# Performance work log

Hardware: AMD Instinct MI355X
Metric: run time of the kernel (lower is better)

Reference implementation:

```python
import jax, jax.numpy as jnp
import numpy as np

T, S, D, W = 256, 512, 640, 64  # tasks, n_support, feat_dim, n_way

def setup_inputs() -> dict:
    key = jax.random.key(0)
    k1, = jax.random.split(key, 1)
    support = jax.random.normal(k1, (T, S, D), dtype=jnp.float32)
    # balanced labels: each class appears exactly S // W times per task
    support_labels = jnp.tile(jnp.arange(S, dtype=jnp.int64) % W, (T, 1))
    return {
        "support": support,
        "support_labels": support_labels,
        "n_way": W,
        "target_pos": jnp.ones((1,), dtype=jnp.float32),
        "target_neg": jnp.zeros((1,), dtype=jnp.float32),
    }

def reference(support, support_labels, n_way, target_pos, target_neg):
    tasks, n_support, _ = support.shape
    # [T, W, S] one-hot (class x support sample)
    one_hot_label = jax.nn.one_hot(support_labels, n_way, dtype=support.dtype)
    one_hot_label = jnp.transpose(one_hot_label, (0, 2, 1))
    # per-class feature sums: [T, W, D] (segment-sum expressed as matmul, as in source)
    pos_feat = jnp.einsum('tws,tsd->twd', one_hot_label, support)
    neg_feat = jnp.sum(support, axis=1, keepdims=True) - pos_feat
    k_shot = jnp.sum(one_hot_label, axis=-1).reshape(tasks, n_way, 1)  # [T, W, 1]
    pos_feat = pos_feat / k_shot
    neg_feat = neg_feat / (n_support - k_shot)
    ff = jnp.sum(pos_feat * pos_feat, axis=2, keepdims=True)
    bb = jnp.sum(neg_feat * neg_feat, axis=2, keepdims=True)
    fb = jnp.sum(pos_feat * neg_feat, axis=2, keepdims=True)
    den = jnp.clip(ff * bb - fb * fb, 1e-06, None)
    fg_scale = target_pos * bb - target_neg * fb
    bg_scale = target_pos * fb - target_neg * ff
    weights = (fg_scale * pos_feat - bg_scale * neg_feat) / den
    return weights
```

## Files before the change

kernel.cpp:

```cpp
#include <hip/hip_runtime.h>

#define T_  256
#define S_  512
#define D_  640
#define W_  64
#define D4  (D_/4)
#define KSH (S_/W_)

static __device__ __forceinline__ float4 f4add(float4 a, float4 b) {
    return make_float4(a.x + b.x, a.y + b.y, a.z + b.z, a.w + b.w);
}

__global__ __launch_bounds__(S_) void k0_build_idx(const int* __restrict__ labels,
                                                   int* __restrict__ idx,
                                                   int* __restrict__ kshot) {
    __shared__ int cnt[W_];
    const int t   = blockIdx.x;
    const int tid = threadIdx.x;
    if (tid < W_) cnt[tid] = 0;
    __syncthreads();
    const int lab  = labels[t * S_ + tid];
    const int slot = atomicAdd(&cnt[lab], 1);
    if (slot < KSH) idx[t * S_ + lab * KSH + slot] = tid;
    __syncthreads();
    if (tid < W_) kshot[t * W_ + tid] = cnt[tid];
}

__global__ __launch_bounds__(320) void k1_pos_sums(const float4* __restrict__ sup4,
                                                   const int* __restrict__ idx,
                                                   const int* __restrict__ kshot,
                                                   float4* __restrict__ out4) {
    const int b   = blockIdx.x;
    const int t   = b / (W_ / 2);
    const int wp  = b % (W_ / 2);
    const int tid = threadIdx.x;
    const int wl  = (tid >= D4) ? 1 : 0;
    const int q   = tid - wl * D4;
    const int w   = wp * 2 + wl;

    const int*    myidx = idx + t * S_ + w * KSH;
    const float4* base  = sup4 + (size_t)t * S_ * D4;
    int ks = kshot[t * W_ + w];
    if (ks > KSH) ks = KSH;

    float4 acc = make_float4(0.f, 0.f, 0.f, 0.f);
    for (int k = 0; k < ks; ++k) {
        const int s = myidx[k];
        acc = f4add(acc, base[(size_t)s * D4 + q]);
    }
    out4[((size_t)t * W_ + w) * D4 + q] = acc;
}

__global__ __launch_bounds__(256) void k2_totals(const float4* __restrict__ pos4,
                                                 float4* __restrict__ tot4) {
    const int gid = blockIdx.x * blockDim.x + threadIdx.x;
    if (gid >= T_ * D4) return;
    const int t = gid / D4;
    const int q = gid - t * D4;
    const float4* base = pos4 + (size_t)t * W_ * D4 + q;
    float4 acc = make_float4(0.f, 0.f, 0.f, 0.f);
#pragma unroll 8
    for (int w = 0; w < W_; ++w) acc = f4add(acc, base[(size_t)w * D4]);
    tot4[gid] = acc;
}

__global__ __launch_bounds__(64) void k3_final(float4* __restrict__ out4,
                                               const float4* __restrict__ tot4,
                                               const int* __restrict__ kshot,
                                               const float* __restrict__ tp_,
                                               const float* __restrict__ tn_) {
    const int b    = blockIdx.x;
    const int t    = b / W_;
    const int w    = b - t * W_;
    const int lane = threadIdx.x;

    const float tp  = tp_[0];
    const float tn  = tn_[0];
    const float ksf = (float)kshot[t * W_ + w];
    const float nkf = (float)S_ - ksf;

    float4 pv[3], nv[3];
    float ff = 0.f, bb = 0.f, fb = 0.f;

#pragma unroll
    for (int r = 0; r < 3; ++r) {
        const int q = lane + r * 64;
        if (q < D4) {
            const float4 p  = out4[((size_t)t * W_ + w) * D4 + q];
            const float4 tv = tot4[(size_t)t * D4 + q];
            float4 pos, neg;
            pos.x = p.x / ksf;  pos.y = p.y / ksf;
            pos.z = p.z / ksf;  pos.w = p.w / ksf;
            neg.x = (tv.x - p.x) / nkf;  neg.y = (tv.y - p.y) / nkf;
            neg.z = (tv.z - p.z) / nkf;  neg.w = (tv.w - p.w) / nkf;
            pv[r] = pos; nv[r] = neg;
            ff += pos.x * pos.x + pos.y * pos.y + pos.z * pos.z + pos.w * pos.w;
            bb += neg.x * neg.x + neg.y * neg.y + neg.z * neg.z + neg.w * neg.w;
            fb += pos.x * neg.x + pos.y * neg.y + pos.z * neg.z + pos.w * neg.w;
        }
    }

#pragma unroll
    for (int off = 32; off > 0; off >>= 1) {
        ff += __shfl_xor(ff, off, 64);
        bb += __shfl_xor(bb, off, 64);
        fb += __shfl_xor(fb, off, 64);
    }

    const float den = fmaxf(ff * bb - fb * fb, 1e-6f);
    const float fg  = tp * bb - tn * fb;
    const float bg  = tp * fb - tn * ff;

#pragma unroll
    for (int r = 0; r < 3; ++r) {
        const int q = lane + r * 64;
        if (q < D4) {
            float4 res;
            res.x = (fg * pv[r].x - bg * nv[r].x) / den;
            res.y = (fg * pv[r].y - bg * nv[r].y) / den;
            res.z = (fg * pv[r].z - bg * nv[r].z) / den;
            res.w = (fg * pv[r].w - bg * nv[r].w) / den;
            out4[((size_t)t * W_ + w) * D4 + q] = res;
        }
    }
}

extern "C" void kernel_launch(void* const* d_in, const int* in_sizes, int n_in,
                              void* d_out, int out_size, void* d_ws, size_t ws_size,
                              hipStream_t stream) {
    const float* support = (const float*)d_in[0];
    const int*   labels  = (const int*)d_in[1];
    const float* tp = (const float*)d_in[3];
    const float* tn = (const float*)d_in[4];
    float* out = (float*)d_out;

    char* ws     = (char*)d_ws;
    int*  idx    = (int*)ws;
    int*  kshot  = (int*)(ws + 512 * 1024);
    float* totals = (float*)(ws + 576 * 1024);

    k0_build_idx<<<T_, S_, 0, stream>>>(labels, idx, kshot);
    k1_pos_sums<<<T_ * (W_ / 2), 320, 0, stream>>>((const float4*)support, idx, kshot,
                                                   (float4*)out);
    k2_totals<<<(T_ * D4 + 255) / 256, 256, 0, stream>>>((const float4*)out,
                                                         (float4*)totals);
    k3_final<<<T_ * W_, 64, 0, stream>>>((float4*)out, (const float4*)totals,
                                         kshot, tp, tn);
}
```

Baseline: 489.6 us.

## Fuse index build, class sums, totals and weight solve into one per-task kernel

Replaces the four-kernel pipeline with one kernel that runs a 1024-thread block per task. Each wave accumulates four classes in registers, the per-task totals come from a shared-memory reduction, and the normalised weights are written directly. This removes the global round trips for the index, the counts, the totals and the intermediate positive sums, plus three kernel launches. The trade-off is only 256 blocks with heavy register and shared-memory use (launch_bounds 1024,1), which may limit latency hiding. Loads also become scalar and strided by 64 instead of float4.

```diff
diff --git a/kernel.cpp b/kernel.cpp
--- a/kernel.cpp
+++ b/kernel.cpp
@@ -1,126 +1,108 @@
 #include <hip/hip_runtime.h>
 
-#define T_  256
-#define S_  512
-#define D_  640
-#define W_  64
-#define D4  (D_/4)
-#define KSH (S_/W_)
+#define T_    256
+#define S_    512
+#define D_    640
+#define W_    64
+#define KSH   8
+#define NWAVE 16
+#define CPW   4
+#define NCOL  10
 
-static __device__ __forceinline__ float4 f4add(float4 a, float4 b) {
-    return make_float4(a.x + b.x, a.y + b.y, a.z + b.z, a.w + b.w);
-}
+__global__ __launch_bounds__(1024, 1) void winit_fused(
+    const float* __restrict__ support,
+    const int* __restrict__ labels,
+    const float* __restrict__ tp_,
+    const float* __restrict__ tn_,
+    float* __restrict__ out) {
+    __shared__ int   cnt[W_];
+    __shared__ int   sidx[W_ * KSH];
+    __shared__ float partial[NWAVE][D_];
+    __shared__ float totals[D_];
 
-__global__ __launch_bounds__(S_) void k0_build_idx(const int* __restrict__ labels,
-                                                   int* __restrict__ idx,
-                                                   int* __restrict__ kshot) {
-    __shared__ int cnt[W_];
-    const int t   = blockIdx.x;
-    const int tid = threadIdx.x;
+    const int t    = blockIdx.x;
+    const int tid  = threadIdx.x;
+    const int wave = tid >> 6;
+    const int lane = tid & 63;
+
     if (tid < W_) cnt[tid] = 0;
     __syncthreads();
-    const int lab  = labels[t * S_ + tid];
-    const int slot = atomicAdd(&cnt[lab], 1);
-    if (slot < KSH) idx[t * S_ + lab * KSH + slot] = tid;
+    if (tid < S_) {
+        const int lab  = labels[t * S_ + tid];
+        const int slot = atomicAdd(&cnt[lab], 1);
+        if (slot < KSH) sidx[lab * KSH + slot] = tid;
+    }
     __syncthreads();
-    if (tid < W_) kshot[t * W_ + tid] = cnt[tid];
-}
 
-__global__ __launch_bounds__(320) void k1_pos_sums(const float4* __restrict__ sup4,
-                                                   const int* __restrict__ idx,
-                                                   const int* __restrict__ kshot,
-                                                   float4* __restrict__ out4) {
-    const int b   = blockIdx.x;
-    const int t   = b / (W_ / 2);
-    const int wp  = b % (W_ / 2);
-    const int tid = threadIdx.x;
-    const int wl  = (tid >= D4) ? 1 : 0;
-    const int q   = tid - wl * D4;
-    const int w   = wp * 2 + wl;
+    const float* base = support + (size_t)t * S_ * D_;
 
-    const int*    myidx = idx + t * S_ + w * KSH;
-    const float4* base  = sup4 + (size_t)t * S_ * D4;
-    int ks = kshot[t * W_ + w];
-    if (ks > KSH) ks = KSH;
-
-    float4 acc = make_float4(0.f, 0.f, 0.f, 0.f);
-    for (int k = 0; k < ks; ++k) {
-        const int s = myidx[k];
-        acc = f4add(acc, base[(size_t)s * D4 + q]);
-    }
-    out4[((size_t)t * W_ + w) * D4 + q] = acc;
-}
-
-__global__ __launch_bounds__(256) void k2_totals(const float4* __restrict__ pos4,
-                                                 float4* __restrict__ tot4) {
-    const int gid = blockIdx.x * blockDim.x + threadIdx.x;
-    if (gid >= T_ * D4) return;
-    const int t = gid / D4;
-    const int q = gid - t * D4;
-    const float4* base = pos4 + (size_t)t * W_ * D4 + q;
-    float4 acc = make_float4(0.f, 0.f, 0.f, 0.f);
-#pragma unroll 8
-    for (int w = 0; w < W_; ++w) acc = f4add(acc, base[(size_t)w * D4]);
-    tot4[gid] = acc;
-}
-
-__global__ __launch_bounds__(64) void k3_final(float4* __restrict__ out4,
-                                               const float4* __restrict__ tot4,
-                                               const int* __restrict__ kshot,
-                                               const float* __restrict__ tp_,
-                                               const float* __restrict__ tn_) {
-    const int b    = blockIdx.x;
-    const int t    = b / W_;
-    const int w    = b - t * W_;
-    const int lane = threadIdx.x;
-
-    const float tp  = tp_[0];
-    const float tn  = tn_[0];
-    const float ksf = (float)kshot[t * W_ + w];
-    const float nkf = (float)S_ - ksf;
-
-    float4 pv[3], nv[3];
-    float ff = 0.f, bb = 0.f, fb = 0.f;
+    float acc[CPW][NCOL];
+#pragma unroll
+    for (int c = 0; c < CPW; ++c)
+#pragma unroll
+        for (int i = 0; i < NCOL; ++i) acc[c][i] = 0.f;
 
 #pragma unroll
-    for (int r = 0; r < 3; ++r) {
-        const int q = lane + r * 64;
-        if (q < D4) {
-            const float4 p  = out4[((size_t)t * W_ + w) * D4 + q];
-            const float4 tv = tot4[(size_t)t * D4 + q];
-            float4 pos, neg;
-            pos.x = p.x / ksf;  pos.y = p.y / ksf;
-            pos.z = p.z / ksf;  pos.w = p.w / ksf;
-            neg.x = (tv.x - p.x) / nkf;  neg.y = (tv.y - p.y) / nkf;
-            neg.z = (tv.z - p.z) / nkf;  neg.w = (tv.w - p.w) / nkf;
-            pv[r] = pos; nv[r] = neg;
-            ff += pos.x * pos.x + pos.y * pos.y + pos.z * pos.z + pos.w * pos.w;
-            bb += neg.x * neg.x + neg.y * neg.y + neg.z * neg.z + neg.w * neg.w;
-            fb += pos.x * neg.x + pos.y * neg.y + pos.z * neg.z + pos.w * neg.w;
+    for (int c = 0; c < CPW; ++c) {
+        const int w  = wave * CPW + c;
+        const int ks = min(cnt[w], KSH);
+        for (int k = 0; k < ks; ++k) {
+            const float* row = base + (size_t)sidx[w * KSH + k] * D_ + lane;
+#pragma unroll
+            for (int i = 0; i < NCOL; ++i) acc[c][i] += row[i * 64];
         }
     }
 
 #pragma unroll
-    for (int off = 32; off > 0; off >>= 1) {
-        ff += __shfl_xor(ff, off, 64);
-        bb += __shfl_xor(bb, off, 64);
-        fb += __shfl_xor(fb, off, 64);
+    for (int i = 0; i < NCOL; ++i)
+        partial[wave][lane + i * 64] = acc[0][i] + acc[1][i] + acc[2][i] + acc[3][i];
+    __syncthreads();
+    if (tid < D_) {
+        float s = 0.f;
+#pragma unroll
+        for (int v = 0; v < NWAVE; ++v) s += partial[v][tid];
+        totals[tid] = s;
     }
+    __syncthreads();
 
-    const float den = fmaxf(ff * bb - fb * fb, 1e-6f);
-    const float fg  = tp * bb - tn * fb;
-    const float bg  = tp * fb - tn * ff;
+    const float tp = tp_[0];
+    const float tn = tn_[0];
 
 #pragma unroll
-    for (int r = 0; r < 3; ++r) {
-        const int q = lane + r * 64;
-        if (q < D4) {
-            float4 res;
-            res.x = (fg * pv[r].x - bg * nv[r].x) / den;
-            res.y = (fg * pv[r].y - bg * nv[r].y) / den;
-            res.z = (fg * pv[r].z - bg * nv[r].z) / den;
-            res.w = (fg * pv[r].w - bg * nv[r].w) / den;
-            out4[((size_t)t * W_ + w) * D4 + q] = res;
+    for (int c = 0; c < CPW; ++c) {
+        const int   w   = wave * CPW + c;
+        const float ksf = (float)cnt[w];
+        const float rks = 1.f / ksf;
+        const float rnk = 1.f / ((float)S_ - ksf);
+
+        float ff = 0.f, bb = 0.f, fb = 0.f;
+#pragma unroll
+        for (int i = 0; i < NCOL; ++i) {
+            const float a  = acc[c][i];
+            const float ps = a * rks;
+            const float ns = (totals[lane + i * 64] - a) * rnk;
+            ff += ps * ps;
+            bb += ns * ns;
+            fb += ps * ns;
+        }
+#pragma unroll
+        for (int off = 32; off > 0; off >>= 1) {
+            ff += __shfl_xor(ff, off, 64);
+            bb += __shfl_xor(bb, off, 64);
+            fb += __shfl_xor(fb, off, 64);
+        }
+        const float den  = fmaxf(ff * bb - fb * fb, 1e-6f);
+        const float rden = 1.f / den;
+        const float fg   = tp * bb - tn * fb;
+        const float bg   = tp * fb - tn * ff;
+
+        float* orow = out + ((size_t)t * W_ + w) * D_ + lane;
+#pragma unroll
+        for (int i = 0; i < NCOL; ++i) {
+            const float a  = acc[c][i];
+            const float ps = a * rks;
+            const float ns = (totals[lane + i * 64] - a) * rnk;
+            orow[i * 64] = (fg * ps - bg * ns) * rden;
         }
     }
 }
@@ -134,16 +116,5 @@
     const float* tn = (const float*)d_in[4];
     float* out = (float*)d_out;
 
-    char* ws     = (char*)d_ws;
-    int*  idx    = (int*)ws;
-    int*  kshot  = (int*)(ws + 512 * 1024);
-    float* totals = (float*)(ws + 576 * 1024);
-
-    k0_build_idx<<<T_, S_, 0, stream>>>(labels, idx, kshot);
-    k1_pos_sums<<<T_ * (W_ / 2), 320, 0, stream>>>((const float4*)support, idx, kshot,
-                                                   (float4*)out);
-    k2_totals<<<(T_ * D4 + 255) / 256, 256, 0, stream>>>((const float4*)out,
-                                                         (float4*)totals);
-    k3_final<<<T_ * W_, 64, 0, stream>>>((float4*)out, (const float4*)totals,
-                                         kshot, tp, tn);
+    winit_fused<<<T_, 1024, 0, stream>>>(support, labels, tp, tn, out);
 }
```

Result: faster. 463.9 us (-5.3%).
